# Optimization experiments

Hardware: AMD Instinct MI355X
Metric: run time of the kernel (lower is better)

The kernel has to match this reference:

```python
import jax, jax.numpy as jnp
import numpy as np

B, C, H, W = 4, 128, 128, 128
HEADS, DHEAD = 8, C // 8
N = H * W
NEG_SLOPE = 0.2
LN_EPS = 1e-5


def _build_grid_edges(h, w):
    # 3x3 neighborhood including self (matches the torch double loop),
    # then append N extra self loops (add_self_loops in the module).
    rows, cols = [], []
    for r in range(h):
        for c in range(w):
            idx = r * w + c
            for dr in (-1, 0, 1):
                for dc in (-1, 0, 1):
                    nr, nc = r + dr, c + dc
                    if 0 <= nr < h and 0 <= nc < w:
                        rows.append(idx)
                        cols.append(nr * w + nc)
    rows += list(range(h * w))
    cols += list(range(h * w))
    return np.asarray(rows, np.int32), np.asarray(cols, np.int32)

_SRC_NP, _DST_NP = _build_grid_edges(H, W)  # PyG: messages flow src -> dst
SRC = jnp.asarray(_SRC_NP)
DST = jnp.asarray(_DST_NP)


def setup_inputs() -> dict:
    key = jax.random.key(0)
    ks = jax.random.split(key, 7)
    s_lin = 1.0 / np.sqrt(C)
    return {
        "x": jax.random.normal(ks[0], (B, C, H, W), jnp.float32),
        "W_lin": jax.random.normal(ks[1], (C, HEADS * DHEAD), jnp.float32) * s_lin,
        "att_src": jax.random.normal(ks[2], (HEADS, DHEAD), jnp.float32) * s_lin,
        "att_dst": jax.random.normal(ks[3], (HEADS, DHEAD), jnp.float32) * s_lin,
        "bias": jnp.zeros((C,), jnp.float32),
        "gamma": jnp.ones((C,), jnp.float32),
        "beta": jnp.zeros((C,), jnp.float32),
    }


def _gat_forward(x, W_lin, att_src, att_dst, bias, gamma, beta):
    b = x.shape[0]
    x_nodes = x.reshape(b, C, N).transpose(0, 2, 1)            # [B,N,C]
    xp = (x_nodes @ W_lin).reshape(b, N, HEADS, DHEAD)          # [B,N,H,D]
    a_src = jnp.einsum('bnhd,hd->bnh', xp, att_src)             # [B,N,H]
    a_dst = jnp.einsum('bnhd,hd->bnh', xp, att_dst)
    score = jax.nn.leaky_relu(a_src[:, SRC] + a_dst[:, DST], NEG_SLOPE)  # [B,E,H]

    def seg_softmax(s):  # [E,H] softmax over edges grouped by DST
        m = jax.ops.segment_max(s, DST, num_segments=N)
        e = jnp.exp(s - m[DST])
        den = jax.ops.segment_sum(e, DST, num_segments=N)
        return e / den[DST]

    alpha = jax.vmap(seg_softmax)(score)                        # [B,E,H]
    msg = xp[:, SRC] * alpha[..., None]                         # [B,E,H,D]
    agg = jax.vmap(lambda m: jax.ops.segment_sum(m, DST, num_segments=N))(msg)
    out = agg.reshape(b, N, C) + bias                           # GATConv bias
    out = jax.nn.elu(out)
    # LayerNorm over channel dim
    mu = out.mean(-1, keepdims=True)
    var = out.var(-1, keepdims=True)
    out = (out - mu) * jax.lax.rsqrt(var + LN_EPS) * gamma + beta
    return out.transpose(0, 2, 1).reshape(b, C, H, W)


def reference(x, W_lin, att_src, att_dst, bias, gamma, beta):
    return _gat_forward(x, W_lin, att_src, att_dst, bias, gamma, beta)
```

## Files before the change

kernel.cpp:

```cpp
#include <hip/hip_runtime.h>
#include <hip/hip_fp16.h>
#include <stdint.h>

#define BATCH  4
#define CCH    128
#define GRID_H 128
#define GRID_W 128
#define NNODE  (GRID_H*GRID_W)
#define NHEAD  8
#define DH     16
#define WPAD   68
#define WROWS  144

typedef __attribute__((ext_vector_type(8))) short short8;
typedef __attribute__((ext_vector_type(4))) float f32x4;
typedef __attribute__((ext_vector_type(4))) unsigned u32x4;

__device__ inline unsigned packbf(float a, float b){
    unsigned r;
    asm("v_cvt_pk_bf16_f32 %0, %1, %2" : "=v"(r) : "v"(a), "v"(b));
    return r;
}
__device__ inline unsigned packhf(float a, float b){
    unsigned r;
    asm("v_cvt_pkrtz_f16_f32 %0, %1, %2" : "=v"(r) : "v"(a), "v"(b));
    return r;
}

__global__ void kW(const float* __restrict__ Wl, const float* __restrict__ attS,
                   const float* __restrict__ attD, unsigned* __restrict__ Wb)
{
    __shared__ float Wa[8][16];
    const int t = threadIdx.x;
    const int cbase = blockIdx.x * 8;
    if (t < 128){
        int cl = t >> 4, j = t & 15;
        const float* av = (j < 8 ? attS + j*DH : attD + (j-8)*DH);
        const float* wr = Wl + (size_t)(cbase + cl)*CCH + (j & 7)*DH;
        float s = 0.f;
        #pragma unroll
        for (int d = 0; d < DH; ++d) s += wr[d]*av[d];
        Wa[cl][j] = s;
    }
    __syncthreads();
    for (int it = 0; it < 3; ++it){
        int flat = it*256 + t;
        if (flat < 576){
            int k2l = flat / 144, co = flat % 144;
            int k2 = blockIdx.x*4 + k2l;
            float w0, w1;
            if (co < CCH){
                w0 = Wl[(size_t)(2*k2)*CCH + co];
                w1 = Wl[(size_t)(2*k2+1)*CCH + co];
            } else {
                w0 = Wa[2*k2l][co-CCH];
                w1 = Wa[2*k2l+1][co-CCH];
            }
            Wb[co*WPAD + k2] = packbf(w0, w1);
        }
    }
}

__global__ __launch_bounds__(256, 3) void kA(
    const float* __restrict__ x, const unsigned* __restrict__ Wbg,
    __half* __restrict__ xpb, float* __restrict__ scS, float* __restrict__ scD)
{
    __shared__ __align__(16) unsigned WbL[WROWS*WPAD];

    const int t  = threadIdx.x;
    const int b  = blockIdx.y;
    const int bx = blockIdx.x;
    const int row = (bx & 7)*16 + (bx >> 3);
    const int n0  = row * GRID_W;

    #pragma unroll
    for (int it = 0; it < 10; ++it){
        int f4 = it*256 + t;
        if (f4 < (WROWS*WPAD)/4)
            *(u32x4*)(&WbL[f4*4]) = *(const u32x4*)(Wbg + (size_t)f4*4);
    }
    __syncthreads();

    const int w = t >> 6, lane = t & 63;
    const int col = lane & 15, q = lane >> 4;
    const float* xb = x + (size_t)b*CCH*NNODE;
    const int nA = n0 + (2*w+0)*16 + col;
    const int nB = n0 + (2*w+1)*16 + col;

    f32x4 acc[2][9];
    #pragma unroll
    for (int mi = 0; mi < 2; ++mi)
        #pragma unroll
        for (int ct = 0; ct < 9; ++ct) acc[mi][ct] = (f32x4)(0.f);

    float xrA[8], xrB[8], x2A[8], x2B[8];
    #pragma unroll
    for (int j = 0; j < 8; ++j){
        const size_t co = (size_t)(q*8 + j)*NNODE;
        xrA[j] = xb[co + nA];
        xrB[j] = xb[co + nB];
    }

    union U { u32x4 u; short8 s; };
    #pragma unroll
    for (int kc = 0; kc < 4; ++kc){
        if (kc < 3){
            #pragma unroll
            for (int j = 0; j < 8; ++j){
                const size_t co = (size_t)((kc+1)*32 + q*8 + j)*NNODE;
                x2A[j] = xb[co + nA];
                x2B[j] = xb[co + nB];
            }
        }
        U fa0, fa1;
        #pragma unroll
        for (int i = 0; i < 4; ++i){
            fa0.u[i] = packbf(xrA[2*i], xrA[2*i+1]);
            fa1.u[i] = packbf(xrB[2*i], xrB[2*i+1]);
        }
        const int kof = kc*16 + q*4;
        #pragma unroll
        for (int ct = 0; ct < 9; ++ct){
            U fb; fb.u = *(const u32x4*)(&WbL[(ct*16+col)*WPAD + kof]);
            acc[0][ct] = __builtin_amdgcn_mfma_f32_16x16x32_bf16(fa0.s, fb.s, acc[0][ct], 0, 0, 0);
            acc[1][ct] = __builtin_amdgcn_mfma_f32_16x16x32_bf16(fa1.s, fb.s, acc[1][ct], 0, 0, 0);
        }
        #pragma unroll
        for (int j = 0; j < 8; ++j){ xrA[j] = x2A[j]; xrB[j] = x2B[j]; }
    }

    __half* xr = xpb + (size_t)b*NNODE*CCH;
    float*  sS = scS + (size_t)b*NNODE*NHEAD;
    float*  sD = scD + (size_t)b*NNODE*NHEAD;
    #pragma unroll
    for (int mi = 0; mi < 2; ++mi){
        #pragma unroll
        for (int r = 0; r < 4; ++r){
            const int n = n0 + (2*w+mi)*16 + q*4 + r;
            #pragma unroll
            for (int ct = 0; ct < 8; ++ct)
                xr[(size_t)n*CCH + ct*16 + col] = __float2half(acc[mi][ct][r]);
            const float v = acc[mi][8][r];
            if (col < 8) sS[(size_t)n*NHEAD + col]     = v;
            else         sD[(size_t)n*NHEAD + col - 8] = v;
        }
    }
}

__device__ inline void kb_issue(int n, const float* __restrict__ scSb,
                                const float* __restrict__ scDb,
                                const uint2* __restrict__ xvb, int h, int l2,
                                int* vm, float aS[9], float* aD, uint2 xv[9])
{
    const int rr = n >> 7, cc = n & 127;
    const bool vU = rr > 0, vD = rr < GRID_H-1, vL = cc > 0, vR = cc < GRID_W-1;
    int m = 0;
    #pragma unroll
    for (int e = 0; e < 9; ++e){
        const int dr = e/3 - 1, dc = e%3 - 1;
        const bool vr_ = (dr < 0) ? vU : (dr > 0 ? vD : true);
        const bool vc_ = (dc < 0) ? vL : (dc > 0 ? vR : true);
        const bool v = vr_ && vc_;
        const int src = v ? (n + dr*GRID_W + dc) : n;
        m |= ((int)v) << e;
        aS[e] = scSb[src*NHEAD + h];
        xv[e] = xvb[(size_t)src*32 + l2];
    }
    *aD = scDb[n*NHEAD + h];
    *vm = m;
}

__global__ __launch_bounds__(256, 4) void kB(
    const __half* __restrict__ xpb, const float* __restrict__ scS,
    const float* __restrict__ scD,
    const float* __restrict__ bias, const float* __restrict__ gamma,
    const float* __restrict__ beta, float* __restrict__ out)
{
    __shared__ float outT[CCH][65];
    const int t = threadIdx.x, w = t >> 6, lane = t & 63;
    const int h2 = lane >> 5, l2 = lane & 31;
    const int b  = blockIdx.y;
    const int bx = blockIdx.x;
    const int xcd = bx & 7, rest = bx >> 3;
    const int hlf = rest & 1, rowin = rest >> 1;
    const int n0  = (xcd*16 + rowin)*GRID_W + hlf*64;

    const uint2* xvb  = (const uint2*)(xpb + (size_t)b*NNODE*CCH);
    const float* scSb = scS + (size_t)b*NNODE*NHEAD;
    const float* scDb = scD + (size_t)b*NNODE*NHEAD;
    const int h = l2 >> 2;
    const f32x4 bi = *(const f32x4*)(bias  + 4*l2);
    const f32x4 ga = *(const f32x4*)(gamma + 4*l2);
    const f32x4 be = *(const f32x4*)(beta  + 4*l2);

    float aSP[2][9]; uint2 xvP[2][9]; float aDP[2]; int vmP[2];

    #define NODE(i) (n0 + w*16 + 2*(i) + h2)
    kb_issue(NODE(0), scSb, scDb, xvb, h, l2, &vmP[0], aSP[0], &aDP[0], xvP[0]);

    #pragma unroll
    for (int ii = 0; ii < 4; ++ii){
        #pragma unroll
        for (int ph = 0; ph < 2; ++ph){
            const int i = 2*ii + ph;
            const int cur = i & 1;
            if (i + 1 < 8)
                kb_issue(NODE(i+1), scSb, scDb, xvb, h, l2,
                         &vmP[cur^1], aSP[cur^1], &aDP[cur^1], xvP[cur^1]);

            const int vm = vmP[cur];
            const float* aS = aSP[cur];
            const uint2*  xv = xvP[cur];
            const float ad = aDP[cur];
            const int nl = w*16 + 2*i + h2;

            float s[9], mx = -1e30f;
            #pragma unroll
            for (int e = 0; e < 9; ++e){
                float sv = aS[e] + ad;
                sv = fmaxf(sv, 0.2f*sv);
                s[e] = ((vm >> e) & 1) ? sv : -1e30f;
                mx = fmaxf(mx, s[e]);
            }
            float wt[9], den = 0.f;
            #pragma unroll
            for (int e = 0; e < 9; ++e){
                float ex = __expf(s[e] - mx);
                ex = ((vm >> e) & 1) ? ex : 0.f;
                wt[e] = ex; den += ex;
            }
            den += wt[4];
            const float inv = __builtin_amdgcn_rcpf(den);

            union HU { unsigned u; __half2 h; };
            HU a01, a23; a01.u = 0u; a23.u = 0u;
            #pragma unroll
            for (int e = 0; e < 9; ++e){
                float f = wt[e] * inv;
                if (e == 4) f += f;
                HU hf; hf.u = packhf(f, f);
                HU lo; lo.u = xv[e].x;
                HU hi; hi.u = xv[e].y;
                a01.h = __hfma2(hf.h, lo.h, a01.h);
                a23.h = __hfma2(hf.h, hi.h, a23.h);
            }
            const float a0 = __low2float(a01.h), a1 = __high2float(a01.h);
            const float a2 = __low2float(a23.h), a3 = __high2float(a23.h);

            float o0 = a0 + bi[0], o1 = a1 + bi[1], o2 = a2 + bi[2], o3 = a3 + bi[3];
            o0 = o0 > 0.f ? o0 : __expf(o0) - 1.f;
            o1 = o1 > 0.f ? o1 : __expf(o1) - 1.f;
            o2 = o2 > 0.f ? o2 : __expf(o2) - 1.f;
            o3 = o3 > 0.f ? o3 : __expf(o3) - 1.f;

            float sm = (o0 + o1) + (o2 + o3);
            float sq = o0*o0 + o1*o1 + o2*o2 + o3*o3;
            #pragma unroll
            for (int off = 1; off <= 16; off <<= 1){
                sm += __shfl_xor(sm, off, 64);
                sq += __shfl_xor(sq, off, 64);
            }
            const float mu  = sm * (1.f/128.f);
            float var = sq * (1.f/128.f) - mu*mu;
            var = var < 0.f ? 0.f : var;
            const float rstd = __builtin_amdgcn_rsqf(var + 1e-5f);
            outT[4*l2+0][nl] = (o0 - mu)*rstd*ga[0] + be[0];
            outT[4*l2+1][nl] = (o1 - mu)*rstd*ga[1] + be[1];
            outT[4*l2+2][nl] = (o2 - mu)*rstd*ga[2] + be[2];
            outT[4*l2+3][nl] = (o3 - mu)*rstd*ga[3] + be[3];
        }
    }
    #undef NODE
    __syncthreads();

    float* ob = out + (size_t)b*CCH*NNODE + n0;
    #pragma unroll
    for (int it = 0; it < 32; ++it){
        int c = it*4 + w;
        ob[(size_t)c*NNODE + lane] = outT[c][lane];
    }
}

extern "C" void kernel_launch(void* const* d_in, const int* in_sizes, int n_in,
                              void* d_out, int out_size, void* d_ws, size_t ws_size,
                              hipStream_t stream)
{
    const float* x    = (const float*)d_in[0];
    const float* Wl   = (const float*)d_in[1];
    const float* attS = (const float*)d_in[2];
    const float* attD = (const float*)d_in[3];
    const float* bias = (const float*)d_in[4];
    const float* gamma= (const float*)d_in[5];
    const float* beta = (const float*)d_in[6];
    float* out = (float*)d_out;

    __half* xpb = (__half*)d_ws;
    float*  scS = (float*)((char*)d_ws + (size_t)BATCH*NNODE*CCH*2);
    float*  scD = scS + (size_t)BATCH*NNODE*NHEAD;
    unsigned* Wb = (unsigned*)(scD + (size_t)BATCH*NNODE*NHEAD);

    kW<<<dim3(16),               256, 0, stream>>>(Wl, attS, attD, Wb);
    kA<<<dim3(NNODE/128, BATCH), 256, 0, stream>>>(x, Wb, xpb, scS, scD);
    kB<<<dim3(NNODE/64,  BATCH), 256, 0, stream>>>(xpb, scS, scD, bias, gamma, beta, out);
}
```

Before: 117.9 us.

## Stage x tile through LDS with vectorized loads before MFMA projection

Kernel kA now loads its x tile for each row with 16-byte vector loads, cooperatively across the block. It packs the values to bf16 pairs and stores them in a padded LDS buffer. The MFMA loop then reads its A fragments from LDS instead of doing scalar strided global loads per lane. This is meant to improve global load coalescing and cut the number of load instructions, but it adds about 35KB of LDS and lowers the occupancy hint from 3 to 2 blocks.

After: 120.4 us. 2.1% more time.

```diff
diff --git a/kernel.cpp b/kernel.cpp
--- a/kernel.cpp
+++ b/kernel.cpp
@@ -11,6 +11,7 @@
 #define DH     16
 #define WPAD   68
 #define WROWS  144
+#define XAPAD  68
 
 typedef __attribute__((ext_vector_type(8))) short short8;
 typedef __attribute__((ext_vector_type(4))) float f32x4;
@@ -61,17 +62,19 @@
     }
 }
 
-__global__ __launch_bounds__(256, 3) void kA(
+__global__ __launch_bounds__(256, 2) void kA(
     const float* __restrict__ x, const unsigned* __restrict__ Wbg,
     __half* __restrict__ xpb, float* __restrict__ scS, float* __restrict__ scD)
 {
     __shared__ __align__(16) unsigned WbL[WROWS*WPAD];
+    __shared__ __align__(16) unsigned xAl[128*XAPAD];
 
     const int t  = threadIdx.x;
     const int b  = blockIdx.y;
     const int bx = blockIdx.x;
     const int row = (bx & 7)*16 + (bx >> 3);
     const int n0  = row * GRID_W;
+    const float* xb = x + (size_t)b*CCH*NNODE;
 
     #pragma unroll
     for (int it = 0; it < 10; ++it){
@@ -79,13 +82,43 @@
         if (f4 < (WROWS*WPAD)/4)
             *(u32x4*)(&WbL[f4*4]) = *(const u32x4*)(Wbg + (size_t)f4*4);
     }
+
+    {
+        const int cpl = t >> 4;
+        const int ng  = (t & 15) * 8;
+        f32x4 P0[4], P1[4];
+        {
+            const float* r0 = xb + (size_t)(2*cpl)*NNODE + n0 + ng;
+            P0[0] = *(const f32x4*)(r0);
+            P0[1] = *(const f32x4*)(r0 + 4);
+            P0[2] = *(const f32x4*)(r0 + NNODE);
+            P0[3] = *(const f32x4*)(r0 + NNODE + 4);
+        }
+        #pragma unroll
+        for (int p = 0; p < 4; ++p){
+            f32x4* C = (p & 1) ? P1 : P0;
+            f32x4* N = (p & 1) ? P0 : P1;
+            if (p < 3){
+                const float* rn = xb + (size_t)(2*((p+1)*16 + cpl))*NNODE + n0 + ng;
+                N[0] = *(const f32x4*)(rn);
+                N[1] = *(const f32x4*)(rn + 4);
+                N[2] = *(const f32x4*)(rn + NNODE);
+                N[3] = *(const f32x4*)(rn + NNODE + 4);
+            }
+            const int k2 = p*16 + cpl;
+            #pragma unroll
+            for (int i = 0; i < 4; ++i){
+                xAl[(ng+i)  *XAPAD + k2] = packbf(C[0][i], C[2][i]);
+                xAl[(ng+4+i)*XAPAD + k2] = packbf(C[1][i], C[3][i]);
+            }
+        }
+    }
     __syncthreads();
 
     const int w = t >> 6, lane = t & 63;
     const int col = lane & 15, q = lane >> 4;
-    const float* xb = x + (size_t)b*CCH*NNODE;
-    const int nA = n0 + (2*w+0)*16 + col;
-    const int nB = n0 + (2*w+1)*16 + col;
+    const int nAl = (2*w)*16 + col;
+    const int nBl = nAl + 16;
 
     f32x4 acc[2][9];
     #pragma unroll
@@ -93,40 +126,19 @@
         #pragma unroll
         for (int ct = 0; ct < 9; ++ct) acc[mi][ct] = (f32x4)(0.f);
 
-    float xrA[8], xrB[8], x2A[8], x2B[8];
-    #pragma unroll
-    for (int j = 0; j < 8; ++j){
-        const size_t co = (size_t)(q*8 + j)*NNODE;
-        xrA[j] = xb[co + nA];
-        xrB[j] = xb[co + nB];
-    }
-
     union U { u32x4 u; short8 s; };
     #pragma unroll
     for (int kc = 0; kc < 4; ++kc){
-        if (kc < 3){
-            #pragma unroll
-            for (int j = 0; j < 8; ++j){
-                const size_t co = (size_t)((kc+1)*32 + q*8 + j)*NNODE;
-                x2A[j] = xb[co + nA];
-                x2B[j] = xb[co + nB];
-            }
-        }
+        const int kof = kc*16 + q*4;
         U fa0, fa1;
-        #pragma unroll
-        for (int i = 0; i < 4; ++i){
-            fa0.u[i] = packbf(xrA[2*i], xrA[2*i+1]);
-            fa1.u[i] = packbf(xrB[2*i], xrB[2*i+1]);
-        }
-        const int kof = kc*16 + q*4;
+        fa0.u = *(const u32x4*)&xAl[nAl*XAPAD + kof];
+        fa1.u = *(const u32x4*)&xAl[nBl*XAPAD + kof];
         #pragma unroll
         for (int ct = 0; ct < 9; ++ct){
             U fb; fb.u = *(const u32x4*)(&WbL[(ct*16+col)*WPAD + kof]);
             acc[0][ct] = __builtin_amdgcn_mfma_f32_16x16x32_bf16(fa0.s, fb.s, acc[0][ct], 0, 0, 0);
             acc[1][ct] = __builtin_amdgcn_mfma_f32_16x16x32_bf16(fa1.s, fb.s, acc[1][ct], 0, 0, 0);
         }
-        #pragma unroll
-        for (int j = 0; j < 8; ++j){ xrA[j] = x2A[j]; xrB[j] = x2B[j]; }
     }
 
     __half* xr = xpb + (size_t)b*NNODE*CCH;
```
